# Optimization experiments

Hardware: AMD Instinct MI355X
Metric: run time of the kernel (lower is better)

The kernel has to match this reference:

```python
import jax, jax.numpy as jnp
import numpy as np

# dims per init_kwargs / input_specs
B, C, H, W = 8, 256, 56, 56
K = 3            # kernel_size
S = 1            # stride
D = 1            # dilation
HEAD = 1
MID = int(C * 0.2)   # se_ratio bottleneck = 51
GAIN = float(np.sqrt(2.0))  # calculate_gain('relu')


def setup_inputs() -> dict:
    key = jax.random.key(0)
    ks = jax.random.split(key, 6)
    sc = 0.05
    return {
        "x": jax.random.normal(ks[0], (B, C, H, W), jnp.float32),
        # channel branch: 1x1 convs stored as dense matrices
        "w1": jax.random.normal(ks[1], (MID, C), jnp.float32) * sc,
        "b1": jnp.zeros((MID,), jnp.float32),
        "w2": jax.random.normal(ks[2], (C * K * K, MID), jnp.float32) * sc,
        "b2": jnp.zeros((C * K * K,), jnp.float32),
        # spatial branch: 1x1 conv c -> head*k^2
        "ws": jax.random.normal(ks[3], (HEAD * K * K, C), jnp.float32) * sc,
        "bs": jnp.zeros((HEAD * K * K,), jnp.float32),
        # FilterNorm running_std parameter (channel branch): randn * gain/k
        "fn_std": jax.random.normal(ks[4], (C * K * K,), jnp.float32) * (GAIN / K),
    }


def _ddf_mul(x, cf, sf):
    """Decoupled dynamic filter, 'mul' combine.
    x: (B,C,H,W), cf: (B,C,K,K) channel filter, sf: (B,K*K,Ho,Wo) spatial filter.
    out[b,c,i,j] = sum_{u,v} x[b,c, i*S+(u-(K-1)/2)*D, j*S+(v-(K-1)/2)*D] * cf[b,c,u,v] * sf[b,u*K+v,i,j]
    Accumulate over the K*K taps to avoid materializing the unfolded tensor."""
    p = D * (K - 1) // 2
    xp = jnp.pad(x, ((0, 0), (0, 0), (p, p), (p, p)))
    Ho, Wo = H // S, W // S
    out = jnp.zeros((B, C, Ho, Wo), x.dtype)
    for u in range(K):
        for v in range(K):
            patch = xp[:, :, u * D:u * D + S * Ho:S, v * D:v * D + S * Wo:S]
            out = out + patch * cf[:, :, u, v][:, :, None, None] * sf[:, u * K + v][:, None]
    return out


def reference(x, w1, b1, w2, b2, ws, bs, fn_std):
    # ---- channel branch: SE-style filter generation ----
    pooled = x.mean((2, 3))                                  # (B,C) global avg pool
    y = jax.nn.relu(pooled @ w1.T + b1)                      # (B,MID)
    y = (y @ w2.T + b2).reshape(B, C, K * K)                 # (B,C,K^2)
    # FilterNorm 'channel': normalize over K^2 (torch std -> ddof=1), learned std
    y = (y - y.mean(-1, keepdims=True)) / (y.std(-1, ddof=1, keepdims=True) + 1e-10)
    cf = (y.reshape(B, C * K * K) * fn_std).reshape(B, C, K, K)
    # ---- spatial branch: 1x1 conv (stride S) + FilterNorm 'spatial' ----
    xs = x[:, :, ::S, ::S]
    sf = jnp.einsum('bchw,nc->bnhw', xs, ws) + bs[None, :, None, None]  # (B,K^2,Ho,Wo)
    sf = sf.reshape(B, HEAD, K * K, H // S, W // S)
    sf = (sf - sf.mean(2, keepdims=True)) / (sf.std(2, ddof=1, keepdims=True) + 1e-10)
    sf = sf.reshape(B, HEAD * K * K, H // S, W // S) * (GAIN / K)
    # ---- fused per-pixel gather-multiply-reduce (head=1 -> no group reshape) ----
    return _ddf_mul(x, cf, sf)
```

## Files before the change

kernel.cpp:

```cpp
#include <hip/hip_runtime.h>
#include <math.h>

#define BB   8
#define CC   256
#define HH   56
#define WW   56
#define KK   3
#define MIDN 51
#define NTAP (KK*KK)
#define CKK  (CC*NTAP)
#define HW   (HH*WW)
#define NCH  8
#define CPC  (CC/NCH)
#define PBLK 13
#define NCPB 2
#define XSTR 33

__global__ __launch_bounds__(256) void k_sfpool(const float* __restrict__ x,
                                                const float* __restrict__ ws,
                                                float* __restrict__ partial,
                                                float* __restrict__ poolpart) {
    int blk = blockIdx.x;
    int pb = blk % PBLK;
    int tmp = blk / PBLK;
    int chunk = tmp % NCH;
    int b = tmp / NCH;
    int t = threadIdx.x;
    __shared__ float xs[256 * XSTR];
    __shared__ float wss[NTAP][CPC];
    __shared__ float psum[8][CPC];
    for (int idx = t; idx < NTAP * CPC; idx += 256) {
        int n = idx / CPC, c = idx - n * CPC;
        wss[n][c] = ws[n * CC + chunk * CPC + c];
    }
    const float* xb = x + ((size_t)(b * CC + chunk * CPC)) * HW + pb * 256;
    bool act = (pb * 256 + t < HW);
    #pragma unroll 4
    for (int c = 0; c < CPC; ++c) {
        float v = act ? xb[(size_t)c * HW + t] : 0.f;
        xs[t * XSTR + c] = v;
    }
    __syncthreads();
    {
        int c = t & 31, seg = t >> 5;
        float s = 0.f;
        #pragma unroll 8
        for (int i = 0; i < 32; ++i) s += xs[(seg * 32 + i) * XSTR + c];
        psum[seg][c] = s;
    }
    float acc[NTAP];
    #pragma unroll
    for (int n = 0; n < NTAP; ++n) acc[n] = 0.f;
    #pragma unroll 4
    for (int c = 0; c < CPC; ++c) {
        float xv = xs[t * XSTR + c];
        #pragma unroll
        for (int n = 0; n < NTAP; ++n) acc[n] += xv * wss[n][c];
    }
    if (act) {
        float* pp = partial + ((size_t)((b * NCH + chunk) * NTAP)) * HW + pb * 256 + t;
        #pragma unroll
        for (int n = 0; n < NTAP; ++n) pp[(size_t)n * HW] = acc[n];
    }
    __syncthreads();
    if (t < CPC) {
        float tot = 0.f;
        #pragma unroll
        for (int seg = 0; seg < 8; ++seg) tot += psum[seg][t];
        poolpart[((size_t)((b * NCH + chunk) * PBLK + pb)) * CPC + t] = tot;
    }
}

#define MLPBLK (BB*NCH)
#define W2CHUNK (CPC*NTAP*MIDN)
__global__ __launch_bounds__(256) void k_mlp_sfB(const float* __restrict__ poolpart,
                                                 const float* __restrict__ w1,
                                                 const float* __restrict__ b1,
                                                 const float* __restrict__ w2,
                                                 const float* __restrict__ b2,
                                                 const float* __restrict__ fn_std,
                                                 const float* __restrict__ partial,
                                                 const float* __restrict__ bs,
                                                 float* __restrict__ cf,
                                                 float* __restrict__ sf) {
    __shared__ float smem[W2CHUNK + 256 + 64 + CPC * NTAP];
    float* w2s = smem;
    float* ps  = smem + W2CHUNK;
    float* y1  = ps + 256;
    float* y2s = y1 + 64;
    int blk = blockIdx.x;
    int t = threadIdx.x;
    if (blk < MLPBLK) {
        int b = blk >> 3, chunk = blk & 7;
        int c0 = chunk * CPC;
        const float4* w2v = (const float4*)(w2 + (size_t)chunk * W2CHUNK);
        float4* w2s4 = (float4*)w2s;
        for (int i = t; i < W2CHUNK / 4; i += 256) w2s4[i] = w2v[i];
        {
            int chunkp = t >> 5, cl = t & 31;
            float s = 0.f;
            const float* pp = poolpart + ((size_t)(b * NCH + chunkp) * PBLK) * CPC + cl;
            #pragma unroll
            for (int pb = 0; pb < PBLK; ++pb) s += pp[pb * CPC];
            ps[t] = s * (1.0f / HW);
        }
        __syncthreads();
        if (t < MIDN) {
            float acc = b1[t];
            const float* wr = w1 + t * CC;
            for (int c2 = 0; c2 < CC; ++c2) acc += ps[c2] * wr[c2];
            y1[t] = fmaxf(acc, 0.f);
        }
        __syncthreads();
        #pragma unroll
        for (int base = 0; base < 512; base += 256) {
            int idx = base + t;
            if (idx < CPC * NTAP) {
                float acc = b2[c0 * NTAP + idx];
                const float* r = w2s + idx * MIDN;
                #pragma unroll 3
                for (int m = 0; m < MIDN; ++m) acc += y1[m] * r[m];
                y2s[idx] = acc;
            }
        }
        __syncthreads();
        if (t < CPC) {
            int c = c0 + t;
            float y2[NTAP];
            #pragma unroll
            for (int q = 0; q < NTAP; ++q) y2[q] = y2s[t * NTAP + q];
            float mean = 0.f;
            #pragma unroll
            for (int q = 0; q < NTAP; ++q) mean += y2[q];
            mean *= (1.f / NTAP);
            float var = 0.f;
            #pragma unroll
            for (int q = 0; q < NTAP; ++q) { float d = y2[q] - mean; var += d * d; }
            float inv = 1.f / (sqrtf(var * (1.f / (NTAP - 1))) + 1e-10f);
            #pragma unroll
            for (int q = 0; q < NTAP; ++q) {
                int idx = c * NTAP + q;
                cf[(size_t)b * CKK + idx] = (y2[q] - mean) * inv * fn_std[idx];
            }
        }
    } else {
        int sblk = blk - MLPBLK;
        int b = sblk / PBLK, pb = sblk % PBLK;
        int p = pb * 256 + t;
        if (p >= HW) return;
        float acc[NTAP];
        #pragma unroll
        for (int n = 0; n < NTAP; ++n) acc[n] = bs[n];
        const float* pp = partial + ((size_t)(b * NCH)) * NTAP * HW + p;
        for (int chunk = 0; chunk < NCH; ++chunk)
            #pragma unroll
            for (int n = 0; n < NTAP; ++n)
                acc[n] += pp[((size_t)(chunk * NTAP + n)) * HW];
        float mean = 0.f;
        #pragma unroll
        for (int n = 0; n < NTAP; ++n) mean += acc[n];
        mean *= (1.f / NTAP);
        float var = 0.f;
        #pragma unroll
        for (int n = 0; n < NTAP; ++n) { float d = acc[n] - mean; var += d * d; }
        float inv = 0.47140452079103173f /
                    (sqrtf(var * (1.f / (NTAP - 1))) + 1e-10f);
        #pragma unroll
        for (int n = 0; n < NTAP; ++n)
            sf[((size_t)(b * NTAP + n)) * HW + p] = (acc[n] - mean) * inv;
    }
}

__global__ __launch_bounds__(256) void k_ddf(const float* __restrict__ x,
                                             const float* __restrict__ cf,
                                             const float* __restrict__ sf,
                                             float* __restrict__ out) {
    int blk = blockIdx.x;
    int b = blk / (CC / NCPB), cg = blk % (CC / NCPB);
    int c0 = cg * NCPB;
    int t = threadIdx.x;
    __shared__ float xt[NCPB][58 * 58];
    for (int idx = t; idx < NCPB * 58 * 58; idx += 256) ((float*)xt)[idx] = 0.f;
    __syncthreads();
    const float* xp = x + ((size_t)(b * CC + c0)) * HW;
    for (int idx = t; idx < HW; idx += 256) {
        int r = idx / WW, col = idx - r * WW;
        int o = (r + 1) * 58 + col + 1;
        xt[0][o] = xp[idx];
        xt[1][o] = xp[HW + idx];
    }
    float cf9[NCPB][NTAP];
    const float* cfp = cf + (size_t)b * CKK + c0 * NTAP;
    #pragma unroll
    for (int k = 0; k < NCPB; ++k)
        #pragma unroll
        for (int n = 0; n < NTAP; ++n) cf9[k][n] = cfp[k * NTAP + n];
    __syncthreads();
    const float* sfb = sf + (size_t)b * NTAP * HW;
    float* op = out + ((size_t)(b * CC + c0)) * HW;
    for (int idx = t; idx < HW; idx += 256) {
        int i = idx / WW, j = idx - i * WW;
        float s9[NTAP];
        #pragma unroll
        for (int n = 0; n < NTAP; ++n) s9[n] = sfb[(size_t)n * HW + idx];
        float acc0 = 0.f, acc1 = 0.f;
        #pragma unroll
        for (int u = 0; u < KK; ++u)
            #pragma unroll
            for (int v = 0; v < KK; ++v) {
                int n = u * KK + v;
                int o = (i + u) * 58 + (j + v);
                acc0 += xt[0][o] * (cf9[0][n] * s9[n]);
                acc1 += xt[1][o] * (cf9[1][n] * s9[n]);
            }
        op[idx] = acc0;
        op[HW + idx] = acc1;
    }
}

extern "C" void kernel_launch(void* const* d_in, const int* in_sizes, int n_in,
                              void* d_out, int out_size, void* d_ws, size_t ws_size,
                              hipStream_t stream) {
    const float* x      = (const float*)d_in[0];
    const float* w1     = (const float*)d_in[1];
    const float* b1     = (const float*)d_in[2];
    const float* w2     = (const float*)d_in[3];
    const float* b2     = (const float*)d_in[4];
    const float* ws     = (const float*)d_in[5];
    const float* bs     = (const float*)d_in[6];
    const float* fn_std = (const float*)d_in[7];
    float* out = (float*)d_out;

    float* wsf      = (float*)d_ws;
    float* cf       = wsf;
    float* sf       = cf + 18432;
    float* poolpart = sf + 225792;
    float* partial  = poolpart + 26624;

    k_sfpool<<<BB * NCH * PBLK, 256, 0, stream>>>(x, ws, partial, poolpart);
    k_mlp_sfB<<<MLPBLK + BB * PBLK, 256, 0, stream>>>(poolpart, w1, b1, w2, b2,
                                                      fn_std, partial, bs, cf, sf);
    k_ddf<<<BB * (CC / NCPB), 256, 0, stream>>>(x, cf, sf, out);
}
```

Before: 126.5 us.

## Process four channels per block in DDF kernel with vectorized float4 tile loads

The DDF kernel now handles four channels per block instead of two, with 512 threads and a generic per-channel accumulator loop. Each spatial-filter load is therefore reused across more channels, which cuts redundant sf reads. Global loads of x into shared memory now use float4. Shared memory per block doubles to about 54KB and the grid halves to 512 blocks, which may lower occupancy.

```diff
diff --git a/kernel.cpp b/kernel.cpp
--- a/kernel.cpp
+++ b/kernel.cpp
@@ -13,7 +13,8 @@
 #define NCH  8
 #define CPC  (CC/NCH)
 #define PBLK 13
-#define NCPB 2
+#define NCPB 4
+#define TILE 3364
 #define XSTR 33
 
 __global__ __launch_bounds__(256) void k_sfpool(const float* __restrict__ x,
@@ -171,7 +172,7 @@
     }
 }
 
-__global__ __launch_bounds__(256) void k_ddf(const float* __restrict__ x,
+__global__ __launch_bounds__(512) void k_ddf(const float* __restrict__ x,
                                              const float* __restrict__ cf,
                                              const float* __restrict__ sf,
                                              float* __restrict__ out) {
@@ -179,15 +180,18 @@
     int b = blk / (CC / NCPB), cg = blk % (CC / NCPB);
     int c0 = cg * NCPB;
     int t = threadIdx.x;
-    __shared__ float xt[NCPB][58 * 58];
-    for (int idx = t; idx < NCPB * 58 * 58; idx += 256) ((float*)xt)[idx] = 0.f;
-    __syncthreads();
-    const float* xp = x + ((size_t)(b * CC + c0)) * HW;
-    for (int idx = t; idx < HW; idx += 256) {
-        int r = idx / WW, col = idx - r * WW;
-        int o = (r + 1) * 58 + col + 1;
-        xt[0][o] = xp[idx];
-        xt[1][o] = xp[HW + idx];
+    __shared__ float xt[NCPB][TILE];
+    for (int idx = t; idx < NCPB * TILE; idx += 512) ((float*)xt)[idx] = 0.f;
+    __syncthreads();
+    const float4* xp4 = (const float4*)(x + ((size_t)(b * CC + c0)) * HW);
+    for (int i4 = t; i4 < NCPB * HW / 4; i4 += 512) {
+        float4 v = xp4[i4];
+        int k = i4 / (HW / 4);
+        int rem4 = i4 - k * (HW / 4);
+        int r = rem4 / (WW / 4);
+        int col = 4 * (rem4 - r * (WW / 4));
+        float* d = &xt[k][(r + 1) * 58 + col + 1];
+        d[0] = v.x; d[1] = v.y; d[2] = v.z; d[3] = v.w;
     }
     float cf9[NCPB][NTAP];
     const float* cfp = cf + (size_t)b * CKK + c0 * NTAP;
@@ -198,23 +202,26 @@
     __syncthreads();
     const float* sfb = sf + (size_t)b * NTAP * HW;
     float* op = out + ((size_t)(b * CC + c0)) * HW;
-    for (int idx = t; idx < HW; idx += 256) {
+    for (int idx = t; idx < HW; idx += 512) {
         int i = idx / WW, j = idx - i * WW;
         float s9[NTAP];
         #pragma unroll
         for (int n = 0; n < NTAP; ++n) s9[n] = sfb[(size_t)n * HW + idx];
-        float acc0 = 0.f, acc1 = 0.f;
+        float acc[NCPB];
+        #pragma unroll
+        for (int k = 0; k < NCPB; ++k) acc[k] = 0.f;
         #pragma unroll
         for (int u = 0; u < KK; ++u)
             #pragma unroll
             for (int v = 0; v < KK; ++v) {
                 int n = u * KK + v;
                 int o = (i + u) * 58 + (j + v);
-                acc0 += xt[0][o] * (cf9[0][n] * s9[n]);
-                acc1 += xt[1][o] * (cf9[1][n] * s9[n]);
+                #pragma unroll
+                for (int k = 0; k < NCPB; ++k)
+                    acc[k] += xt[k][o] * (cf9[k][n] * s9[n]);
             }
-        op[idx] = acc0;
-        op[HW + idx] = acc1;
+        #pragma unroll
+        for (int k = 0; k < NCPB; ++k) op[(size_t)k * HW + idx] = acc[k];
     }
 }
 
@@ -240,5 +247,5 @@
     k_sfpool<<<BB * NCH * PBLK, 256, 0, stream>>>(x, ws, partial, poolpart);
     k_mlp_sfB<<<MLPBLK + BB * PBLK, 256, 0, stream>>>(poolpart, w1, b1, w2, b2,
                                                       fn_std, partial, bs, cf, sf);
-    k_ddf<<<BB * (CC / NCPB), 256, 0, stream>>>(x, cf, sf, out);
-}
+    k_ddf<<<BB * (CC / NCPB), 512, 0, stream>>>(x, cf, sf, out);
+}
```

Result: faster. 123.9 us (-2.0%).
